# Performance work log

Measured on AMD Instinct MI355X. Metric: run time of the kernel, lower is better.

Reference implementation:

```python
import jax, jax.numpy as jnp
import numpy as np

N = 100000   # nodes
E = 3200000  # edges
D = 128      # embedding_dimension


def leaky(x, slope):
    return jnp.where(x >= 0, x, slope * x)


def gat_conv(x, src, dst, lin_w, att_src, att_dst, bias, heads, out_ch):
    """PyG GATConv (concat=True, negative_slope=0.2, add_self_loops handled by caller)."""
    n = x.shape[0]
    h = (x @ lin_w).reshape(n, heads, out_ch)                 # [N,H,C]
    a_s = (h * att_src).sum(-1)                               # [N,H]
    a_d = (h * att_dst).sum(-1)                               # [N,H]
    alpha = leaky(a_s[src] + a_d[dst], 0.2)                   # [E,H]
    # segment softmax over incoming edges of each dst node
    m = jax.ops.segment_max(alpha, dst, num_segments=n)
    ex = jnp.exp(alpha - m[dst])
    s = jax.ops.segment_sum(ex, dst, num_segments=n)
    w = ex / (s[dst] + 1e-16)                                 # [E,H]
    out = jax.ops.segment_sum(h[src] * w[:, :, None], dst, num_segments=n)
    return out.reshape(n, heads * out_ch) + bias


def setup_inputs() -> dict:
    key = jax.random.key(0)
    ks = jax.random.split(key, 32)
    rn = lambda k, s, sc=0.05: jax.random.normal(k, s, dtype=jnp.float32) * sc
    q = D // 4  # 32
    inp = {
        "des": rn(ks[0], (N, 768), 1.0),
        "tweet": rn(ks[1], (N, 768), 1.0),
        "num_prop": rn(ks[2], (N, 6), 1.0),
        "cat_prop": rn(ks[3], (N, 11), 1.0),
        "edge_index": jax.random.randint(ks[4], (2, E), 0, N),
        "edge_type": jax.random.randint(ks[5], (E,), 0, 2),
        # encoder params
        "w_des": rn(ks[6], (768, q)), "b_des": jnp.zeros((q,), jnp.float32),
        "w_tw": rn(ks[7], (768, q)), "b_tw": jnp.zeros((q,), jnp.float32),
        "w_np": rn(ks[8], (6, q)), "b_np": jnp.zeros((q,), jnp.float32),
        "w_cp": rn(ks[9], (11, q)), "b_cp": jnp.zeros((q,), jnp.float32),
        "w_in": rn(ks[10], (D, D)), "b_in": jnp.zeros((D,), jnp.float32),
        # gat1: heads=4, out=32, concat -> 128
        "g1_w": rn(ks[11], (D, 4 * q)), "g1_as": rn(ks[12], (4, q)),
        "g1_ad": rn(ks[13], (4, q)), "g1_b": jnp.zeros((D,), jnp.float32),
        # gat2: heads=1, out=128
        "g2_w": rn(ks[14], (D, D)), "g2_as": rn(ks[15], (1, D)),
        "g2_ad": rn(ks[16], (1, D)), "g2_b": jnp.zeros((D,), jnp.float32),
        # output MLP
        "w_o1": rn(ks[17], (D, D)), "b_o1": jnp.zeros((D,), jnp.float32),
        "w_o2": rn(ks[18], (D, 2)), "b_o2": jnp.zeros((2,), jnp.float32),
    }
    return inp


def reference(des, tweet, num_prop, cat_prop, edge_index, edge_type,
              w_des, b_des, w_tw, b_tw, w_np, b_np, w_cp, b_cp,
              w_in, b_in, g1_w, g1_as, g1_ad, g1_b,
              g2_w, g2_as, g2_ad, g2_b, w_o1, b_o1, w_o2, b_o2):
    # encoders (nn.LeakyReLU default slope = 0.01)
    d = leaky(des @ w_des + b_des, 0.01)
    t = leaky(tweet @ w_tw + b_tw, 0.01)
    n_ = leaky(num_prop @ w_np + b_np, 0.01)
    c = leaky(cat_prop @ w_cp + b_cp, 0.01)
    x = jnp.concatenate([d, t, n_, c], axis=1)          # [N,128]
    x = leaky(x @ w_in + b_in, 0.01)
    # add self-loops (PyG GATConv default add_self_loops=True)
    loop = jnp.arange(N)
    src = jnp.concatenate([edge_index[0], loop])
    dst = jnp.concatenate([edge_index[1], loop])
    x = gat_conv(x, src, dst, g1_w, g1_as, g1_ad, g1_b, 4, D // 4)
    # dropout is identity in eval mode
    x = gat_conv(x, src, dst, g2_w, g2_as, g2_ad, g2_b, 1, D)
    x = leaky(x @ w_o1 + b_o1, 0.01)
    return x @ w_o2 + b_o2                              # [N,2]
```

## Files before the change

### kernel.cpp

```cpp
#include <hip/hip_runtime.h>
#include <hip/hip_bf16.h>

#define DEV_INLINE __device__ __forceinline__

using bf16x8 = __attribute__((ext_vector_type(8))) short;
using f32x4  = __attribute__((ext_vector_type(4))) float;

DEV_INLINE float leaky(float x, float s) { return x >= 0.f ? x : s * x; }
DEV_INLINE float bf2f(unsigned short u) { return __uint_as_float(((unsigned)u) << 16); }
DEV_INLINE unsigned short f2bf(float f) {
  unsigned u = __float_as_uint(f);
  unsigned r = ((u >> 16) & 1u) + 0x7fffu;
  return (unsigned short)((u + r) >> 16);
}

#define BSHIFT 8
#define NBLK   256

__global__ __launch_bounds__(256) void csr_hist_kernel(
    const int* __restrict__ dst, int* __restrict__ blkcnt, int NB, int E) {
  __shared__ int hist[512];
  int blk = blockIdx.x, t = threadIdx.x;
  for (int i = t; i < NB; i += 256) hist[i] = 0;
  __syncthreads();
  int chunk = (E + NBLK - 1) / NBLK;
  int e0 = blk * chunk;
  int e1 = e0 + chunk; if (e1 > E) e1 = E;
  for (int e = e0 + t; e < e1; e += 256)
    atomicAdd(&hist[dst[e] >> BSHIFT], 1);
  __syncthreads();
  for (int i = t; i < NB; i += 256)
    blkcnt[(size_t)blk * NB + i] = hist[i];
}

__global__ __launch_bounds__(1024) void csr_scan_kernel(
    const int* __restrict__ blkcnt, int* __restrict__ blkoff,
    int* __restrict__ sbkt, int NB) {
  __shared__ int sums[1024];
  int M = NB * NBLK;
  int t = threadIdx.x;
  int chunk = (M + 1023) / 1024;
  int lo = t * chunk;
  int hi = lo + chunk; if (hi > M) hi = M;
  int s = 0;
  for (int q = lo; q < hi; ++q) {
    int b = q >> 8, blk = q & (NBLK - 1);
    s += blkcnt[(size_t)blk * NB + b];
  }
  sums[t] = s;
  __syncthreads();
  for (int off = 1; off < 1024; off <<= 1) {
    int v = (t >= off) ? sums[t - off] : 0;
    __syncthreads();
    sums[t] += v;
    __syncthreads();
  }
  int run = (t == 0) ? 0 : sums[t - 1];
  for (int q = lo; q < hi; ++q) {
    int b = q >> 8, blk = q & (NBLK - 1);
    if (blk == 0) sbkt[b] = run;
    blkoff[(size_t)blk * NB + b] = run;
    run += blkcnt[(size_t)blk * NB + b];
  }
  if (lo < M && hi == M) sbkt[NB] = run;
}

__global__ __launch_bounds__(256) void csr_scatter_kernel(
    const int* __restrict__ src, const int* __restrict__ dst,
    const int* __restrict__ blkoff, int* __restrict__ pairs, int NB, int E) {
  __shared__ int cur[512];
  int blk = blockIdx.x, t = threadIdx.x;
  for (int i = t; i < NB; i += 256) cur[i] = blkoff[(size_t)blk * NB + i];
  __syncthreads();
  int chunk = (E + NBLK - 1) / NBLK;
  int e0 = blk * chunk;
  int e1 = e0 + chunk; if (e1 > E) e1 = E;
  for (int e = e0 + t; e < e1; e += 256) {
    int d = dst[e];
    int pos = atomicAdd(&cur[d >> BSHIFT], 1);
    pairs[pos] = (src[e] << BSHIFT) | (d & 255);
  }
}

__global__ __launch_bounds__(256) void bkt_build_kernel(
    const int* __restrict__ sbkt, const int* __restrict__ pairs,
    int* __restrict__ offs, int* __restrict__ csr, int n_rows, int NB) {
  __shared__ int cnt[256];
  __shared__ int cur[256];
  int b = blockIdx.x, t = threadIdx.x;
  int start = sbkt[b];
  int end   = sbkt[b + 1];
  cnt[t] = 0;
  __syncthreads();
  for (int e = start + t; e < end; e += 256)
    atomicAdd(&cnt[pairs[e] & 255], 1);
  __syncthreads();
  for (int off = 1; off < 256; off <<= 1) {
    int v = (t >= off) ? cnt[t - off] : 0;
    __syncthreads();
    cnt[t] += v;
    __syncthreads();
  }
  int ex = (t == 0) ? 0 : cnt[t - 1];
  cur[t] = start + ex;
  int node = (b << BSHIFT) + t;
  if (node < n_rows) offs[node] = start + ex;
  if (t == 0 && b == NB - 1) offs[n_rows] = end;
  __syncthreads();
  for (int e = start + t; e < end; e += 256) {
    int v = pairs[e];
    int pos = atomicAdd(&cur[v & 255], 1);
    csr[pos] = v >> BSHIFT;
  }
}

__global__ __launch_bounds__(256) void swz_kernel(
    const float* __restrict__ w_des, const float* __restrict__ w_tw,
    const float* __restrict__ w_in, const float* __restrict__ g1_w,
    const float* __restrict__ g2_w, const float* __restrict__ w_o1,
    short* __restrict__ o_des, short* __restrict__ o_tw,
    short* __restrict__ o_in, short* __restrict__ o_g1,
    short* __restrict__ o_g2, short* __restrict__ o_o1) {
  const float* W; short* O; int K, COLS;
  switch (blockIdx.y) {
    case 0: W = w_des; O = o_des; K = 768; COLS = 32; break;
    case 1: W = w_tw;  O = o_tw;  K = 768; COLS = 32; break;
    case 2: W = w_in;  O = o_in;  K = 128; COLS = 128; break;
    case 3: W = g1_w;  O = o_g1;  K = 128; COLS = 128; break;
    case 4: W = g2_w;  O = o_g2;  K = 128; COLS = 128; break;
    default: W = w_o1; O = o_o1;  K = 128; COLS = 128; break;
  }
  int CT = COLS >> 4;
  int t = blockIdx.x * 256 + threadIdx.x;
  int total = (K >> 5) * CT * 64;
  if (t >= total) return;
  int L = t & 63;
  int rest = t >> 6;
  int ct = rest % CT;
  int ks = rest / CT;
  int kbase = ks * 32 + (L >> 4) * 8;
  int col = ct * 16 + (L & 15);
  #pragma unroll
  for (int j = 0; j < 8; ++j)
    O[t * 8 + j] = (short)f2bf(W[(size_t)(kbase + j) * COLS + col]);
}

__global__ __launch_bounds__(256) void enc_mfma_kernel(
    const float* __restrict__ des, const float* __restrict__ tweet,
    const short* __restrict__ wsw_des, const short* __restrict__ wsw_tw,
    const float* __restrict__ b_des, const float* __restrict__ b_tw,
    unsigned short* __restrict__ x0, int n_rows) {
  const float* A; const short* Wsw; const float* bias; int col_off;
  if (blockIdx.y == 0) { A = des;   Wsw = wsw_des; bias = b_des; col_off = 0; }
  else                 { A = tweet; Wsw = wsw_tw;  bias = b_tw;  col_off = 32; }
  int wv = threadIdx.x >> 6, lane = threadIdx.x & 63;
  int row0 = blockIdx.x * 64 + wv * 16;
  int rA = row0 + (lane & 15);
  int rc = rA < n_rows ? rA : (n_rows - 1);
  const float* arow = A + (size_t)rc * 768 + ((lane >> 4) * 8);
  f32x4 acc0 = {0.f, 0.f, 0.f, 0.f}, acc1 = {0.f, 0.f, 0.f, 0.f};

  float4 p0a = *(const float4*)(arow + 0);
  float4 p0b = *(const float4*)(arow + 4);
  float4 p1a = *(const float4*)(arow + 32);
  float4 p1b = *(const float4*)(arow + 36);
  #pragma unroll
  for (int ks = 0; ks < 24; ++ks) {
    float4 c0 = p0a, c1 = p0b;
    p0a = p1a; p0b = p1b;
    if (ks + 2 < 24) {
      p1a = *(const float4*)(arow + (ks + 2) * 32);
      p1b = *(const float4*)(arow + (ks + 2) * 32 + 4);
    }
    bf16x8 af;
    af[0] = (short)f2bf(c0.x); af[1] = (short)f2bf(c0.y);
    af[2] = (short)f2bf(c0.z); af[3] = (short)f2bf(c0.w);
    af[4] = (short)f2bf(c1.x); af[5] = (short)f2bf(c1.y);
    af[6] = (short)f2bf(c1.z); af[7] = (short)f2bf(c1.w);
    bf16x8 b0 = *(const bf16x8*)&Wsw[(size_t)((ks * 2 + 0) * 64 + lane) * 8];
    bf16x8 b1 = *(const bf16x8*)&Wsw[(size_t)((ks * 2 + 1) * 64 + lane) * 8];
    acc0 = __builtin_amdgcn_mfma_f32_16x16x32_bf16(af, b0, acc0, 0, 0, 0);
    acc1 = __builtin_amdgcn_mfma_f32_16x16x32_bf16(af, b1, acc1, 0, 0, 0);
  }
  int quad = lane >> 4, cl = lane & 15;
  #pragma unroll
  for (int r = 0; r < 4; ++r) {
    int row = row0 + quad * 4 + r;
    if (row >= n_rows) continue;
    float v0 = leaky(acc0[r] + bias[cl], 0.01f);
    float v1 = leaky(acc1[r] + bias[16 + cl], 0.01f);
    x0[(size_t)row * 128 + col_off + cl]      = f2bf(v0);
    x0[(size_t)row * 128 + col_off + 16 + cl] = f2bf(v1);
  }
}

__global__ __launch_bounds__(256) void enc_small_kernel(
    const float* __restrict__ np_, const float* __restrict__ cp,
    const float* __restrict__ w_np, const float* __restrict__ w_cp,
    const float* __restrict__ b_np, const float* __restrict__ b_cp,
    unsigned short* __restrict__ x0, int n_rows) {
  int gid = blockIdx.x * 256 + threadIdx.x;
  int node = gid >> 6;
  int c = gid & 63;
  if (node >= n_rows) return;
  float acc; int col;
  if (c < 32) {
    acc = b_np[c];
    #pragma unroll
    for (int k = 0; k < 6; ++k) acc += np_[(size_t)node * 6 + k] * w_np[k * 32 + c];
    col = 64 + c;
  } else {
    int cc = c - 32;
    acc = b_cp[cc];
    #pragma unroll
    for (int k = 0; k < 11; ++k) acc += cp[(size_t)node * 11 + k] * w_cp[k * 32 + cc];
    col = 96 + cc;
  }
  x0[(size_t)node * 128 + col] = f2bf(leaky(acc, 0.01f));
}

template <bool LEAKY, bool BIAS>
__global__ __launch_bounds__(256) void dense_mfma_kernel(
    const unsigned short* __restrict__ X, const short* __restrict__ Wsw,
    const float* __restrict__ bias, unsigned short* __restrict__ Y, int n_rows) {
  int wv = threadIdx.x >> 6, lane = threadIdx.x & 63;
  int row0 = blockIdx.x * 64 + wv * 16;
  int rA = row0 + (lane & 15);
  int rc = rA < n_rows ? rA : (n_rows - 1);
  const unsigned short* xr = X + (size_t)rc * 128 + (lane >> 4) * 8;
  f32x4 acc[8] = {};
  #pragma unroll
  for (int ks = 0; ks < 4; ++ks) {
    bf16x8 af = *(const bf16x8*)(xr + ks * 32);
    #pragma unroll
    for (int ct = 0; ct < 8; ++ct) {
      bf16x8 bfr = *(const bf16x8*)&Wsw[(size_t)((ks * 8 + ct) * 64 + lane) * 8];
      acc[ct] = __builtin_amdgcn_mfma_f32_16x16x32_bf16(af, bfr, acc[ct], 0, 0, 0);
    }
  }
  int quad = lane >> 4, cl = lane & 15;
  #pragma unroll
  for (int r = 0; r < 4; ++r) {
    int row = row0 + quad * 4 + r;
    if (row >= n_rows) continue;
    #pragma unroll
    for (int ct = 0; ct < 8; ++ct) {
      float v = acc[ct][r];
      int col = ct * 16 + cl;
      if (BIAS) v += bias[col];
      if (LEAKY) v = leaky(v, 0.01f);
      Y[(size_t)row * 128 + col] = f2bf(v);
    }
  }
}

template <int H>
__global__ __launch_bounds__(256) void att_dots_kernel(
    const ushort2* __restrict__ h2, const float* __restrict__ att_s,
    const float* __restrict__ att_d, float* __restrict__ a_s,
    float* __restrict__ a_d, int n_rows) {
  int wave = (blockIdx.x * 256 + threadIdx.x) >> 6;
  int lane = threadIdx.x & 63;
  if (wave >= n_rows) return;
  int c = lane * 2;
  ushort2 hv2 = h2[(size_t)wave * 64 + lane];
  float hx = bf2f(hv2.x), hy = bf2f(hv2.y);
  float2 sv = *(const float2*)&att_s[c];
  float2 dv = *(const float2*)&att_d[c];
  float ps = hx * sv.x + hy * sv.y;
  float pd = hx * dv.x + hy * dv.y;
  const int G = 64 / H;
  #pragma unroll
  for (int o = 1; o < G; o <<= 1) {
    ps += __shfl_xor(ps, o, 64);
    pd += __shfl_xor(pd, o, 64);
  }
  if ((lane & (G - 1)) == 0) {
    int head = lane / G;
    a_s[(size_t)wave * H + head] = ps;
    a_d[(size_t)wave * H + head] = pd;
  }
}

template <int H>
__global__ __launch_bounds__(256) void agg_kernel(
    const ushort2* __restrict__ h2, const float* __restrict__ a_src,
    const float* __restrict__ a_dst, const int* __restrict__ offs,
    const int* __restrict__ csr_src, const float* __restrict__ bias,
    unsigned short* __restrict__ out, int n_rows) {
  int n = (blockIdx.x * 256 + threadIdx.x) >> 6;
  int lane = threadIdx.x & 63;
  if (n >= n_rows) return;
  int c = lane * 2;
  int head = (c * H) >> 7;

  float ad = a_dst[(size_t)n * H + head];
  float m = leaky(a_src[(size_t)n * H + head] + ad, 0.2f);
  float l = 1.0f;
  ushort2 hv = h2[(size_t)n * 64 + lane];
  float acc0 = bf2f(hv.x), acc1 = bf2f(hv.y);

  int e = offs[n], e1 = offs[n + 1];
  for (; e + 4 <= e1; e += 4) {
    int s0 = csr_src[e], s1 = csr_src[e + 1], s2 = csr_src[e + 2], s3 = csr_src[e + 3];
    float a0 = leaky(a_src[(size_t)s0 * H + head] + ad, 0.2f);
    float a1 = leaky(a_src[(size_t)s1 * H + head] + ad, 0.2f);
    float a2 = leaky(a_src[(size_t)s2 * H + head] + ad, 0.2f);
    float a3 = leaky(a_src[(size_t)s3 * H + head] + ad, 0.2f);
    ushort2 g0 = h2[(size_t)s0 * 64 + lane];
    ushort2 g1 = h2[(size_t)s1 * 64 + lane];
    ushort2 g2 = h2[(size_t)s2 * 64 + lane];
    ushort2 g3 = h2[(size_t)s3 * 64 + lane];
    float mn = fmaxf(fmaxf(fmaxf(a0, a1), fmaxf(a2, a3)), m);
    float sc = __expf(m - mn);
    float x0_ = __expf(a0 - mn), x1_ = __expf(a1 - mn);
    float x2_ = __expf(a2 - mn), x3_ = __expf(a3 - mn);
    l = l * sc + x0_ + x1_ + x2_ + x3_;
    acc0 = acc0 * sc + x0_ * bf2f(g0.x) + x1_ * bf2f(g1.x) + x2_ * bf2f(g2.x) + x3_ * bf2f(g3.x);
    acc1 = acc1 * sc + x0_ * bf2f(g0.y) + x1_ * bf2f(g1.y) + x2_ * bf2f(g2.y) + x3_ * bf2f(g3.y);
    m = mn;
  }
  for (; e < e1; ++e) {
    int s = csr_src[e];
    float a = leaky(a_src[(size_t)s * H + head] + ad, 0.2f);
    float mn = fmaxf(m, a);
    float sc = __expf(m - mn), ex = __expf(a - mn);
    ushort2 g = h2[(size_t)s * 64 + lane];
    l = l * sc + ex;
    acc0 = acc0 * sc + ex * bf2f(g.x);
    acc1 = acc1 * sc + ex * bf2f(g.y);
    m = mn;
  }
  float inv = 1.0f / (l + 1e-16f);
  out[(size_t)n * 128 + c]     = f2bf(acc0 * inv + bias[c]);
  out[(size_t)n * 128 + c + 1] = f2bf(acc1 * inv + bias[c + 1]);
}

__global__ __launch_bounds__(256) void final2_kernel(
    const unsigned short* __restrict__ tt, const float* __restrict__ w,
    const float* __restrict__ b, float* __restrict__ out, int n_rows) {
  int gid = blockIdx.x * 256 + threadIdx.x;
  if (gid >= n_rows) return;
  const uint4* tp = (const uint4*)(tt + (size_t)gid * 128);
  float a0 = b[0], a1 = b[1];
  #pragma unroll 4
  for (int q = 0; q < 16; ++q) {
    uint4 raw = tp[q];
    unsigned vals[4] = {raw.x, raw.y, raw.z, raw.w};
    #pragma unroll
    for (int i = 0; i < 4; ++i) {
      float f0 = bf2f((unsigned short)(vals[i] & 0xffffu));
      float f1 = bf2f((unsigned short)(vals[i] >> 16));
      int k = q * 8 + i * 2;
      a0 += f0 * w[k * 2]     + f1 * w[(k + 1) * 2];
      a1 += f0 * w[k * 2 + 1] + f1 * w[(k + 1) * 2 + 1];
    }
  }
  out[(size_t)gid * 2 + 0] = a0;
  out[(size_t)gid * 2 + 1] = a1;
}

static inline size_t align256(size_t x) { return (x + 255) & ~(size_t)255; }

extern "C" void kernel_launch(void* const* d_in, const int* in_sizes, int n_in,
                              void* d_out, int out_size, void* d_ws, size_t ws_size,
                              hipStream_t stream) {
  const float* des      = (const float*)d_in[0];
  const float* tweet    = (const float*)d_in[1];
  const float* num_prop = (const float*)d_in[2];
  const float* cat_prop = (const float*)d_in[3];
  const int*   ei       = (const int*)d_in[4];
  const float* w_des = (const float*)d_in[6];
  const float* b_des = (const float*)d_in[7];
  const float* w_tw  = (const float*)d_in[8];
  const float* b_tw  = (const float*)d_in[9];
  const float* w_np  = (const float*)d_in[10];
  const float* b_np  = (const float*)d_in[11];
  const float* w_cp  = (const float*)d_in[12];
  const float* b_cp  = (const float*)d_in[13];
  const float* w_in  = (const float*)d_in[14];
  const float* b_in  = (const float*)d_in[15];
  const float* g1_w  = (const float*)d_in[16];
  const float* g1_as = (const float*)d_in[17];
  const float* g1_ad = (const float*)d_in[18];
  const float* g1_b  = (const float*)d_in[19];
  const float* g2_w  = (const float*)d_in[20];
  const float* g2_as = (const float*)d_in[21];
  const float* g2_ad = (const float*)d_in[22];
  const float* g2_b  = (const float*)d_in[23];
  const float* w_o1  = (const float*)d_in[24];
  const float* b_o1  = (const float*)d_in[25];
  const float* w_o2  = (const float*)d_in[26];
  const float* b_o2  = (const float*)d_in[27];

  const int N = in_sizes[0] / 768;
  const int E = in_sizes[4] / 2;
  const int* src = ei;
  const int* dst = ei + E;

  const int NB = (N + 255) >> BSHIFT;

  char* p = (char*)d_ws;
  unsigned short* bufA = (unsigned short*)p; p += align256((size_t)N * 128 * 2);
  unsigned short* bufB = (unsigned short*)p; p += align256((size_t)N * 128 * 2);
  float* as1 = (float*)p; p += align256((size_t)N * 4 * 4);
  float* ad1 = (float*)p; p += align256((size_t)N * 4 * 4);
  float* as2 = (float*)p; p += align256((size_t)N * 4);
  float* ad2 = (float*)p; p += align256((size_t)N * 4);
  int* offs = (int*)p; p += align256((size_t)(N + 1) * 4);
  int* csr  = (int*)p; p += align256((size_t)E * 4);
  short* sw_des = (short*)p; p += align256(768 * 32 * 2);
  short* sw_tw  = (short*)p; p += align256(768 * 32 * 2);
  short* sw_in  = (short*)p; p += align256(128 * 128 * 2);
  short* sw_g1  = (short*)p; p += align256(128 * 128 * 2);
  short* sw_g2  = (short*)p; p += align256(128 * 128 * 2);
  short* sw_o1  = (short*)p; p += align256(128 * 128 * 2);

  int* pairs = (int*)bufA;
  char* q = (char*)bufB;
  int* blkcnt = (int*)q; q += align256((size_t)NBLK * NB * 4);
  int* blkoff = (int*)q; q += align256((size_t)NBLK * NB * 4);
  int* sbkt   = (int*)q; q += align256((size_t)(NB + 1) * 4);

  dim3 gswz(12, 6);
  swz_kernel<<<gswz, 256, 0, stream>>>(w_des, w_tw, w_in, g1_w, g2_w, w_o1,
                                       sw_des, sw_tw, sw_in, sw_g1, sw_g2, sw_o1);

  csr_hist_kernel<<<NBLK, 256, 0, stream>>>(dst, blkcnt, NB, E);
  csr_scan_kernel<<<1, 1024, 0, stream>>>(blkcnt, blkoff, sbkt, NB);
  csr_scatter_kernel<<<NBLK, 256, 0, stream>>>(src, dst, blkoff, pairs, NB, E);
  bkt_build_kernel<<<NB, 256, 0, stream>>>(sbkt, pairs, offs, csr, N, NB);

  dim3 genc((N + 63) / 64, 2);
  enc_mfma_kernel<<<genc, 256, 0, stream>>>(des, tweet, sw_des, sw_tw, b_des, b_tw, bufA, N);
  enc_small_kernel<<<((size_t)N * 64 + 255) / 256, 256, 0, stream>>>(
      num_prop, cat_prop, w_np, w_cp, b_np, b_cp, bufA, N);

  int gd = (N + 63) / 64;
  int gw = ((size_t)N * 64 + 255) / 256;

  dense_mfma_kernel<true, true><<<gd, 256, 0, stream>>>(bufA, sw_in, b_in, bufB, N);

  dense_mfma_kernel<false, false><<<gd, 256, 0, stream>>>(bufB, sw_g1, nullptr, bufA, N);
  att_dots_kernel<4><<<gw, 256, 0, stream>>>((const ushort2*)bufA, g1_as, g1_ad, as1, ad1, N);
  agg_kernel<4><<<gw, 256, 0, stream>>>((const ushort2*)bufA, as1, ad1, offs, csr, g1_b, bufB, N);

  dense_mfma_kernel<false, false><<<gd, 256, 0, stream>>>(bufB, sw_g2, nullptr, bufA, N);
  att_dots_kernel<1><<<gw, 256, 0, stream>>>((const ushort2*)bufA, g2_as, g2_ad, as2, ad2, N);
  agg_kernel<1><<<gw, 256, 0, stream>>>((const ushort2*)bufA, as2, ad2, offs, csr, g2_b, bufB, N);

  dense_mfma_kernel<true, true><<<gd, 256, 0, stream>>>(bufB, sw_o1, b_o1, bufA, N);
  final2_kernel<<<(N + 255) / 256, 256, 0, stream>>>(bufA, w_o2, b_o2, (float*)d_out, N);
}
```

Baseline: 1.353 ms.

## Fuse dense GEMMs with attention dots and output head into epilogues

Merges the input linear and the GAT1 projection into one kernel by staging the intermediate tile in swizzled LDS, and computes the per-head attention dot products inside the GEMM epilogue. The GAT2 projection likewise computes its attention dots in the epilogue, and the final 128x2 projection is folded into the output MLP kernel. This removes several kernel launches and full N×128 bf16 round-trips through global memory, at the cost of extra cross-lane shuffle reductions and a less general kernel structure.

```diff
diff --git a/kernel.cpp b/kernel.cpp
--- a/kernel.cpp
+++ b/kernel.cpp
@@ -12,6 +12,11 @@
   unsigned u = __float_as_uint(f);
   unsigned r = ((u >> 16) & 1u) + 0x7fffu;
   return (unsigned short)((u + r) >> 16);
+}
+DEV_INLINE float red16(float v) {
+  v += __shfl_xor(v, 1, 64); v += __shfl_xor(v, 2, 64);
+  v += __shfl_xor(v, 4, 64); v += __shfl_xor(v, 8, 64);
+  return v;
 }
 
 #define BSHIFT 8
@@ -219,66 +224,170 @@
   x0[(size_t)node * 128 + col] = f2bf(leaky(acc, 0.01f));
 }
 
-template <bool LEAKY, bool BIAS>
-__global__ __launch_bounds__(256) void dense_mfma_kernel(
-    const unsigned short* __restrict__ X, const short* __restrict__ Wsw,
-    const float* __restrict__ bias, unsigned short* __restrict__ Y, int n_rows) {
+__global__ __launch_bounds__(256) void h1_fused_kernel(
+    const unsigned short* __restrict__ X, const short* __restrict__ sw_in,
+    const float* __restrict__ b_in, const short* __restrict__ sw_g1,
+    const float* __restrict__ att_s, const float* __restrict__ att_d,
+    unsigned short* __restrict__ H1, float* __restrict__ a_s,
+    float* __restrict__ a_d, int n_rows) {
+  __shared__ char xt[4 * 4096];
   int wv = threadIdx.x >> 6, lane = threadIdx.x & 63;
   int row0 = blockIdx.x * 64 + wv * 16;
   int rA = row0 + (lane & 15);
   int rc = rA < n_rows ? rA : (n_rows - 1);
   const unsigned short* xr = X + (size_t)rc * 128 + (lane >> 4) * 8;
+  int quad = lane >> 4, cl = lane & 15;
+  char* xw = xt + wv * 4096;
+
   f32x4 acc[8] = {};
   #pragma unroll
   for (int ks = 0; ks < 4; ++ks) {
     bf16x8 af = *(const bf16x8*)(xr + ks * 32);
     #pragma unroll
     for (int ct = 0; ct < 8; ++ct) {
+      bf16x8 bfr = *(const bf16x8*)&sw_in[(size_t)((ks * 8 + ct) * 64 + lane) * 8];
+      acc[ct] = __builtin_amdgcn_mfma_f32_16x16x32_bf16(af, bfr, acc[ct], 0, 0, 0);
+    }
+  }
+  #pragma unroll
+  for (int r = 0; r < 4; ++r) {
+    int lr = quad * 4 + r;
+    #pragma unroll
+    for (int ct = 0; ct < 8; ++ct) {
+      float v = leaky(acc[ct][r] + b_in[ct * 16 + cl], 0.01f);
+      int cb = (ct * 32 + cl * 2) ^ ((lr & 7) << 4);
+      *(unsigned short*)(xw + lr * 256 + cb) = f2bf(v);
+    }
+  }
+  f32x4 acc2[8] = {};
+  int lr2 = lane & 15;
+  #pragma unroll
+  for (int ks = 0; ks < 4; ++ks) {
+    int cb0 = (((lane >> 4) * 16 + ks * 64)) ^ ((lr2 & 7) << 4);
+    bf16x8 af = *(const bf16x8*)(xw + lr2 * 256 + cb0);
+    #pragma unroll
+    for (int ct = 0; ct < 8; ++ct) {
+      bf16x8 bfr = *(const bf16x8*)&sw_g1[(size_t)((ks * 8 + ct) * 64 + lane) * 8];
+      acc2[ct] = __builtin_amdgcn_mfma_f32_16x16x32_bf16(af, bfr, acc2[ct], 0, 0, 0);
+    }
+  }
+  float asv[8], adv[8];
+  #pragma unroll
+  for (int ct = 0; ct < 8; ++ct) {
+    int idx = (ct >> 1) * 32 + (ct & 1) * 16 + cl;
+    asv[ct] = att_s[idx];
+    adv[ct] = att_d[idx];
+  }
+  #pragma unroll
+  for (int r = 0; r < 4; ++r) {
+    int row = row0 + quad * 4 + r;
+    bool ok = row < n_rows;
+    if (ok) {
+      #pragma unroll
+      for (int ct = 0; ct < 8; ++ct)
+        H1[(size_t)row * 128 + ct * 16 + cl] = f2bf(acc2[ct][r]);
+    }
+    #pragma unroll
+    for (int h = 0; h < 4; ++h) {
+      float ps = acc2[2 * h][r] * asv[2 * h] + acc2[2 * h + 1][r] * asv[2 * h + 1];
+      float pd = acc2[2 * h][r] * adv[2 * h] + acc2[2 * h + 1][r] * adv[2 * h + 1];
+      ps = red16(ps); pd = red16(pd);
+      if (ok && cl == 0) {
+        a_s[(size_t)row * 4 + h] = ps;
+        a_d[(size_t)row * 4 + h] = pd;
+      }
+    }
+  }
+}
+
+__global__ __launch_bounds__(256) void h2_fused_kernel(
+    const unsigned short* __restrict__ X, const short* __restrict__ Wsw,
+    const float* __restrict__ att_s, const float* __restrict__ att_d,
+    unsigned short* __restrict__ H2, float* __restrict__ a_s,
+    float* __restrict__ a_d, int n_rows) {
+  int wv = threadIdx.x >> 6, lane = threadIdx.x & 63;
+  int row0 = blockIdx.x * 64 + wv * 16;
+  int rA = row0 + (lane & 15);
+  int rc = rA < n_rows ? rA : (n_rows - 1);
+  const unsigned short* xr = X + (size_t)rc * 128 + (lane >> 4) * 8;
+  int quad = lane >> 4, cl = lane & 15;
+  f32x4 acc[8] = {};
+  #pragma unroll
+  for (int ks = 0; ks < 4; ++ks) {
+    bf16x8 af = *(const bf16x8*)(xr + ks * 32);
+    #pragma unroll
+    for (int ct = 0; ct < 8; ++ct) {
       bf16x8 bfr = *(const bf16x8*)&Wsw[(size_t)((ks * 8 + ct) * 64 + lane) * 8];
       acc[ct] = __builtin_amdgcn_mfma_f32_16x16x32_bf16(af, bfr, acc[ct], 0, 0, 0);
     }
   }
-  int quad = lane >> 4, cl = lane & 15;
+  float asv[8], adv[8];
+  #pragma unroll
+  for (int ct = 0; ct < 8; ++ct) {
+    asv[ct] = att_s[ct * 16 + cl];
+    adv[ct] = att_d[ct * 16 + cl];
+  }
   #pragma unroll
   for (int r = 0; r < 4; ++r) {
     int row = row0 + quad * 4 + r;
-    if (row >= n_rows) continue;
-    #pragma unroll
-    for (int ct = 0; ct < 8; ++ct) {
-      float v = acc[ct][r];
-      int col = ct * 16 + cl;
-      if (BIAS) v += bias[col];
-      if (LEAKY) v = leaky(v, 0.01f);
-      Y[(size_t)row * 128 + col] = f2bf(v);
-    }
-  }
-}
-
-template <int H>
-__global__ __launch_bounds__(256) void att_dots_kernel(
-    const ushort2* __restrict__ h2, const float* __restrict__ att_s,
-    const float* __restrict__ att_d, float* __restrict__ a_s,
-    float* __restrict__ a_d, int n_rows) {
-  int wave = (blockIdx.x * 256 + threadIdx.x) >> 6;
-  int lane = threadIdx.x & 63;
-  if (wave >= n_rows) return;
-  int c = lane * 2;
-  ushort2 hv2 = h2[(size_t)wave * 64 + lane];
-  float hx = bf2f(hv2.x), hy = bf2f(hv2.y);
-  float2 sv = *(const float2*)&att_s[c];
-  float2 dv = *(const float2*)&att_d[c];
-  float ps = hx * sv.x + hy * sv.y;
-  float pd = hx * dv.x + hy * dv.y;
-  const int G = 64 / H;
-  #pragma unroll
-  for (int o = 1; o < G; o <<= 1) {
-    ps += __shfl_xor(ps, o, 64);
-    pd += __shfl_xor(pd, o, 64);
-  }
-  if ((lane & (G - 1)) == 0) {
-    int head = lane / G;
-    a_s[(size_t)wave * H + head] = ps;
-    a_d[(size_t)wave * H + head] = pd;
+    bool ok = row < n_rows;
+    float ps = 0.f, pd = 0.f;
+    #pragma unroll
+    for (int ct = 0; ct < 8; ++ct) {
+      if (ok) H2[(size_t)row * 128 + ct * 16 + cl] = f2bf(acc[ct][r]);
+      ps += acc[ct][r] * asv[ct];
+      pd += acc[ct][r] * adv[ct];
+    }
+    ps = red16(ps); pd = red16(pd);
+    if (ok && cl == 0) { a_s[row] = ps; a_d[row] = pd; }
+  }
+}
+
+__global__ __launch_bounds__(256) void out_fused_kernel(
+    const unsigned short* __restrict__ X, const short* __restrict__ Wsw,
+    const float* __restrict__ bias, const float* __restrict__ w_o2,
+    const float* __restrict__ b_o2, float* __restrict__ out, int n_rows) {
+  int wv = threadIdx.x >> 6, lane = threadIdx.x & 63;
+  int row0 = blockIdx.x * 64 + wv * 16;
+  int rA = row0 + (lane & 15);
+  int rc = rA < n_rows ? rA : (n_rows - 1);
+  const unsigned short* xr = X + (size_t)rc * 128 + (lane >> 4) * 8;
+  int quad = lane >> 4, cl = lane & 15;
+  f32x4 acc[8] = {};
+  #pragma unroll
+  for (int ks = 0; ks < 4; ++ks) {
+    bf16x8 af = *(const bf16x8*)(xr + ks * 32);
+    #pragma unroll
+    for (int ct = 0; ct < 8; ++ct) {
+      bf16x8 bfr = *(const bf16x8*)&Wsw[(size_t)((ks * 8 + ct) * 64 + lane) * 8];
+      acc[ct] = __builtin_amdgcn_mfma_f32_16x16x32_bf16(af, bfr, acc[ct], 0, 0, 0);
+    }
+  }
+  float w0v[8], w1v[8], bv[8];
+  #pragma unroll
+  for (int ct = 0; ct < 8; ++ct) {
+    int col = ct * 16 + cl;
+    w0v[ct] = w_o2[col * 2 + 0];
+    w1v[ct] = w_o2[col * 2 + 1];
+    bv[ct]  = bias[col];
+  }
+  float ob0 = b_o2[0], ob1 = b_o2[1];
+  #pragma unroll
+  for (int r = 0; r < 4; ++r) {
+    int row = row0 + quad * 4 + r;
+    bool ok = row < n_rows;
+    float p0 = 0.f, p1 = 0.f;
+    #pragma unroll
+    for (int ct = 0; ct < 8; ++ct) {
+      float t = leaky(acc[ct][r] + bv[ct], 0.01f);
+      p0 += t * w0v[ct];
+      p1 += t * w1v[ct];
+    }
+    p0 = red16(p0); p1 = red16(p1);
+    if (ok && cl == 0) {
+      out[(size_t)row * 2 + 0] = p0 + ob0;
+      out[(size_t)row * 2 + 1] = p1 + ob1;
+    }
   }
 }
 
@@ -334,30 +443,6 @@
   float inv = 1.0f / (l + 1e-16f);
   out[(size_t)n * 128 + c]     = f2bf(acc0 * inv + bias[c]);
   out[(size_t)n * 128 + c + 1] = f2bf(acc1 * inv + bias[c + 1]);
-}
-
-__global__ __launch_bounds__(256) void final2_kernel(
-    const unsigned short* __restrict__ tt, const float* __restrict__ w,
-    const float* __restrict__ b, float* __restrict__ out, int n_rows) {
-  int gid = blockIdx.x * 256 + threadIdx.x;
-  if (gid >= n_rows) return;
-  const uint4* tp = (const uint4*)(tt + (size_t)gid * 128);
-  float a0 = b[0], a1 = b[1];
-  #pragma unroll 4
-  for (int q = 0; q < 16; ++q) {
-    uint4 raw = tp[q];
-    unsigned vals[4] = {raw.x, raw.y, raw.z, raw.w};
-    #pragma unroll
-    for (int i = 0; i < 4; ++i) {
-      float f0 = bf2f((unsigned short)(vals[i] & 0xffffu));
-      float f1 = bf2f((unsigned short)(vals[i] >> 16));
-      int k = q * 8 + i * 2;
-      a0 += f0 * w[k * 2]     + f1 * w[(k + 1) * 2];
-      a1 += f0 * w[k * 2 + 1] + f1 * w[(k + 1) * 2 + 1];
-    }
-  }
-  out[(size_t)gid * 2 + 0] = a0;
-  out[(size_t)gid * 2 + 1] = a1;
 }
 
 static inline size_t align256(size_t x) { return (x + 255) & ~(size_t)255; }
@@ -439,16 +524,12 @@
   int gd = (N + 63) / 64;
   int gw = ((size_t)N * 64 + 255) / 256;
 
-  dense_mfma_kernel<true, true><<<gd, 256, 0, stream>>>(bufA, sw_in, b_in, bufB, N);
-
-  dense_mfma_kernel<false, false><<<gd, 256, 0, stream>>>(bufB, sw_g1, nullptr, bufA, N);
-  att_dots_kernel<4><<<gw, 256, 0, stream>>>((const ushort2*)bufA, g1_as, g1_ad, as1, ad1, N);
-  agg_kernel<4><<<gw, 256, 0, stream>>>((const ushort2*)bufA, as1, ad1, offs, csr, g1_b, bufB, N);
-
-  dense_mfma_kernel<false, false><<<gd, 256, 0, stream>>>(bufB, sw_g2, nullptr, bufA, N);
-  att_dots_kernel<1><<<gw, 256, 0, stream>>>((const ushort2*)bufA, g2_as, g2_ad, as2, ad2, N);
-  agg_kernel<1><<<gw, 256, 0, stream>>>((const ushort2*)bufA, as2, ad2, offs, csr, g2_b, bufB, N);
-
-  dense_mfma_kernel<true, true><<<gd, 256, 0, stream>>>(bufB, sw_o1, b_o1, bufA, N);
-  final2_kernel<<<(N + 255) / 256, 256, 0, stream>>>(bufA, w_o2, b_o2, (float*)d_out, N);
-}
+  h1_fused_kernel<<<gd, 256, 0, stream>>>(bufA, sw_in, b_in, sw_g1,
+                                          g1_as, g1_ad, bufB, as1, ad1, N);
+  agg_kernel<4><<<gw, 256, 0, stream>>>((const ushort2*)bufB, as1, ad1, offs, csr, g1_b, bufA, N);
+
+  h2_fused_kernel<<<gd, 256, 0, stream>>>(bufA, sw_g2, g2_as, g2_ad, bufB, as2, ad2, N);
+  agg_kernel<1><<<gw, 256, 0, stream>>>((const ushort2*)bufB, as2, ad2, offs, csr, g2_b, bufA, N);
+
+  out_fused_kernel<<<gd, 256, 0, stream>>>(bufA, sw_o1, b_o1, w_o2, b_o2, (float*)d_out, N);
+}
```

Result: faster. 1.311 ms (-3.1%).
